# Kernel tuning notes

Measured on AMD Instinct MI355X. Metric: run time of the kernel, lower is better.

Reference implementation:

```python
import jax, jax.numpy as jnp
import numpy as np

B, N_CAM, D_BINS, HF, WF, C = 1, 6, 118, 32, 88, 80
DZ, DY, DX = 1, 128, 128
N_POINTS = 1_000_000
BEV_FEAT_SHAPE = (B, DZ, DY, DX, C)  # (B, Dz, Dy, Dx, C)


def setup_inputs() -> dict:
    key = jax.random.key(0)
    k1, k2, k3, k4, k5 = jax.random.split(key, 5)
    depth = jax.random.uniform(k1, (B, N_CAM, D_BINS, HF, WF), dtype=jnp.float32)
    feat = jax.random.normal(k2, (B, N_CAM, HF, WF, C), dtype=jnp.float32)
    n_depth = B * N_CAM * D_BINS * HF * WF      # flattened depth size
    n_feat_rows = B * N_CAM * HF * WF           # rows of flattened feat
    n_bev = B * DZ * DY * DX                    # flattened BEV grid size
    ranks_depths = jax.random.randint(k3, (N_POINTS,), 0, n_depth, dtype=jnp.int32)
    ranks_feats = jax.random.randint(k4, (N_POINTS,), 0, n_feat_rows, dtype=jnp.int32)
    ranks_bevs = jnp.sort(jax.random.randint(k5, (N_POINTS,), 0, n_bev, dtype=jnp.int32))
    # intervals consistent with sorted ranks_bevs (contiguous runs of equal bev rank)
    rb = np.asarray(ranks_bevs)
    change = np.concatenate([[True], rb[1:] != rb[:-1]])
    starts = np.flatnonzero(change)
    lengths = np.diff(np.append(starts, len(rb)))
    return {
        "depth": depth,
        "feat": feat,
        "ranks_depths": ranks_depths,
        "ranks_feats": ranks_feats,
        "ranks_bevs": ranks_bevs,
        "bev_feat_shape": BEV_FEAT_SHAPE,
        "interval_starts": jnp.asarray(starts, dtype=jnp.int32),
        "interval_lengths": jnp.asarray(lengths, dtype=jnp.int32),
    }


def reference(depth, feat, ranks_depths, ranks_feats, ranks_bevs,
              bev_feat_shape, interval_starts, interval_lengths):
    # bev_pool_v2: gather depth scalar and feat row per point, multiply,
    # scatter-sum into the BEV grid. Interval-based summation over sorted
    # ranks_bevs is mathematically a segment-sum keyed by ranks_bevs, so we
    # use segment_sum directly (intervals are redundant metadata).
    b, dz, dy, dx, c = bev_feat_shape
    d = depth.reshape(-1)[ranks_depths]               # [P]
    f = feat.reshape(-1, c)[ranks_feats]              # [P, C]
    out = jax.ops.segment_sum(f * d[:, None], ranks_bevs,
                              num_segments=b * dz * dy * dx)  # [B*Dz*Dy*Dx, C]
    out = out.reshape(b, dz, dy, dx, c)
    return jnp.transpose(out, (0, 4, 1, 2, 3))        # (B, C, Dz, Dy, Dx)
```

## Files before the change

### kernel.cpp

```cpp
#include <hip/hip_runtime.h>
#include <hip/hip_bf16.h>


#define C_CH   80
#define NL     10
#define SPLITS 8
#define IPB    4
#define BLOCK  (IPB * SPLITS * NL)

__global__ void prep_kernel(const float*  __restrict__ depth,
                            const int*    __restrict__ rd,
                            const float4* __restrict__ feat4,
                            float* __restrict__ dgath,
                            uint2* __restrict__ fbf,
                            int P, int NF4) {
    int i = blockIdx.x * blockDim.x + threadIdx.x;
    if (i < NF4) {
        float4 v = feat4[i];
        float f[4] = {v.x, v.y, v.z, v.w};
        unsigned h[4];
        #pragma unroll
        for (int k = 0; k < 4; ++k) {
            unsigned u = __float_as_uint(f[k]);
            h[k] = (u + 0x7fffu + ((u >> 16) & 1u)) >> 16;
        }
        uint2 o;
        o.x = h[0] | (h[1] << 16);
        o.y = h[2] | (h[3] << 16);
        fbf[i] = o;
    }
    if (i < P) dgath[i] = depth[rd[i]];
}

__device__ __forceinline__ void bf8_fma(float acc[8], float d, int4 w) {
    unsigned v[4] = {(unsigned)w.x, (unsigned)w.y, (unsigned)w.z, (unsigned)w.w};
    #pragma unroll
    for (int k = 0; k < 4; ++k) {
        float lo = __uint_as_float(v[k] << 16);
        float hi = __uint_as_float(v[k] & 0xffff0000u);
        acc[2 * k]     += d * lo;
        acc[2 * k + 1] += d * hi;
    }
}

template <bool FAST>
__global__ __launch_bounds__(BLOCK) void bev_main(
    const float*  __restrict__ depth,
    const int*    __restrict__ rd,
    const float*  __restrict__ dgath,
    const int4*   __restrict__ fbf,
    const float4* __restrict__ featf,
    const int*    __restrict__ rf,
    const int*    __restrict__ rb,
    const int*    __restrict__ istart,
    const int*    __restrict__ ilen,
    int n_intervals,
    int n_bev,
    float* __restrict__ out)
{
    __shared__ float red[IPB][SPLITS][NL][9];

    int tid   = threadIdx.x;
    int il    = tid / (SPLITS * NL);
    int r     = tid - il * (SPLITS * NL);
    int split = r / NL;
    int l10   = r - split * NL;
    int interval = blockIdx.x * IPB + il;
    bool valid = interval < n_intervals;

    float acc[8] = {0.f, 0.f, 0.f, 0.f, 0.f, 0.f, 0.f, 0.f};
    int bev = 0;

    if (valid) {
        int start = istart[interval];
        int len   = ilen[interval];
        bev = rb[start];

        int i = split;
        for (; i + SPLITS < len; i += 2 * SPLITS) {
            int p0 = start + i;
            int p1 = p0 + SPLITS;
            float d0 = FAST ? dgath[p0] : depth[rd[p0]];
            float d1 = FAST ? dgath[p1] : depth[rd[p1]];
            int q0 = rf[p0], q1 = rf[p1];
            if (FAST) {
                int4 w0 = fbf[(long)q0 * NL + l10];
                int4 w1 = fbf[(long)q1 * NL + l10];
                bf8_fma(acc, d0, w0);
                bf8_fma(acc, d1, w1);
            } else {
                float4 a0 = featf[(long)q0 * 20 + l10 * 2];
                float4 a1 = featf[(long)q0 * 20 + l10 * 2 + 1];
                float4 b0 = featf[(long)q1 * 20 + l10 * 2];
                float4 b1 = featf[(long)q1 * 20 + l10 * 2 + 1];
                acc[0] += d0 * a0.x; acc[1] += d0 * a0.y;
                acc[2] += d0 * a0.z; acc[3] += d0 * a0.w;
                acc[4] += d0 * a1.x; acc[5] += d0 * a1.y;
                acc[6] += d0 * a1.z; acc[7] += d0 * a1.w;
                acc[0] += d1 * b0.x; acc[1] += d1 * b0.y;
                acc[2] += d1 * b0.z; acc[3] += d1 * b0.w;
                acc[4] += d1 * b1.x; acc[5] += d1 * b1.y;
                acc[6] += d1 * b1.z; acc[7] += d1 * b1.w;
            }
        }
        for (; i < len; i += SPLITS) {
            int p = start + i;
            float d = FAST ? dgath[p] : depth[rd[p]];
            int q = rf[p];
            if (FAST) {
                bf8_fma(acc, d, fbf[(long)q * NL + l10]);
            } else {
                float4 a0 = featf[(long)q * 20 + l10 * 2];
                float4 a1 = featf[(long)q * 20 + l10 * 2 + 1];
                acc[0] += d * a0.x; acc[1] += d * a0.y;
                acc[2] += d * a0.z; acc[3] += d * a0.w;
                acc[4] += d * a1.x; acc[5] += d * a1.y;
                acc[6] += d * a1.z; acc[7] += d * a1.w;
            }
        }
    }

    #pragma unroll
    for (int j = 0; j < 8; ++j) red[il][split][l10][j] = acc[j];
    __syncthreads();

    if (valid && split == 0) {
        float s[8];
        #pragma unroll
        for (int j = 0; j < 8; ++j) s[j] = acc[j];
        #pragma unroll
        for (int k = 1; k < SPLITS; ++k) {
            #pragma unroll
            for (int j = 0; j < 8; ++j) s[j] += red[il][k][l10][j];
        }
        long ob = (long)(l10 * 8) * n_bev + bev;
        #pragma unroll
        for (int j = 0; j < 8; ++j) out[ob + (long)j * n_bev] = s[j];
    }
}

extern "C" void kernel_launch(void* const* d_in, const int* in_sizes, int n_in,
                              void* d_out, int out_size, void* d_ws, size_t ws_size,
                              hipStream_t stream) {
    const float*  depth = (const float*)d_in[0];
    const float4* feat4 = (const float4*)d_in[1];
    const int* ranks_depth = (const int*)d_in[2];
    const int* ranks_feat  = (const int*)d_in[3];
    const int* ranks_bev   = (const int*)d_in[4];
    const int* interval_starts  = (const int*)d_in[6];
    const int* interval_lengths = (const int*)d_in[7];

    int P   = in_sizes[2];
    int NF  = in_sizes[1];
    int NF4 = NF / 4;
    int n_intervals = in_sizes[6];
    int n_bev = out_size / C_CH;
    float* out = (float*)d_out;

    size_t dg_bytes  = ((size_t)P * sizeof(float) + 15) & ~(size_t)15;
    size_t fbf_bytes = (size_t)NF * 2;
    bool fast = ws_size >= dg_bytes + fbf_bytes;

    float* dgath = (float*)d_ws;
    uint2* fbf   = (uint2*)((char*)d_ws + dg_bytes);

    hipMemsetAsync(d_out, 0, (size_t)out_size * sizeof(float), stream);

    if (fast) {
        int n = P > NF4 ? P : NF4;
        int gblock = 256;
        int ggrid = (n + gblock - 1) / gblock;
        prep_kernel<<<ggrid, gblock, 0, stream>>>(depth, ranks_depth, feat4,
                                                  dgath, fbf, P, NF4);
    }

    int grid = (n_intervals + IPB - 1) / IPB;
    if (fast) {
        bev_main<true><<<grid, BLOCK, 0, stream>>>(
            depth, ranks_depth, dgath, (const int4*)fbf, feat4,
            ranks_feat, ranks_bev, interval_starts, interval_lengths,
            n_intervals, n_bev, out);
    } else {
        bev_main<false><<<grid, BLOCK, 0, stream>>>(
            depth, ranks_depth, dgath, (const int4*)fbf, feat4,
            ranks_feat, ranks_bev, interval_starts, interval_lengths,
            n_intervals, n_bev, out);
    }
}
```

Measured before the change: 118.1 us.

## Pack feat index with bf16-rounded depth per point and unroll main loop by four

A new prep stage converts the full depth tensor to bf16. A second prep kernel then gathers the depth for each point and stores it beside that point's feature row index in one 8-byte record. In the main kernel each point needs only one coalesced load before the feature gather, and the inner loop is unrolled four-way to put more gathers in flight. The cost is an extra kernel launch, a full pass over the depth tensor, and depth values rounded to bf16 precision.

```diff
diff --git a/kernel.cpp b/kernel.cpp
--- a/kernel.cpp
+++ b/kernel.cpp
@@ -8,28 +8,34 @@
 #define IPB    4
 #define BLOCK  (IPB * SPLITS * NL)
 
-__global__ void prep_kernel(const float*  __restrict__ depth,
-                            const int*    __restrict__ rd,
-                            const float4* __restrict__ feat4,
-                            float* __restrict__ dgath,
-                            uint2* __restrict__ fbf,
-                            int P, int NF4) {
+__device__ __forceinline__ unsigned pack_bf16(float2 v) {
+    unsigned a = __float_as_uint(v.x);
+    unsigned b = __float_as_uint(v.y);
+    a = (a + 0x7fffu + ((a >> 16) & 1u)) >> 16;
+    b = (b + 0x7fffu + ((b >> 16) & 1u)) >> 16;
+    return a | (b << 16);
+}
+
+__global__ void prep_convert(const float2* __restrict__ feat2,
+                             const float2* __restrict__ depth2,
+                             unsigned* __restrict__ fbf,
+                             unsigned* __restrict__ dbf,
+                             int NF2, int ND2) {
     int i = blockIdx.x * blockDim.x + threadIdx.x;
-    if (i < NF4) {
-        float4 v = feat4[i];
-        float f[4] = {v.x, v.y, v.z, v.w};
-        unsigned h[4];
-        #pragma unroll
-        for (int k = 0; k < 4; ++k) {
-            unsigned u = __float_as_uint(f[k]);
-            h[k] = (u + 0x7fffu + ((u >> 16) & 1u)) >> 16;
-        }
-        uint2 o;
-        o.x = h[0] | (h[1] << 16);
-        o.y = h[2] | (h[3] << 16);
-        fbf[i] = o;
+    if (i < NF2) fbf[i] = pack_bf16(feat2[i]);
+    if (i < ND2) dbf[i] = pack_bf16(depth2[i]);
+}
+
+__global__ void prep_pack(const unsigned short* __restrict__ dbf,
+                          const int* __restrict__ rd,
+                          const int* __restrict__ rf,
+                          uint2* __restrict__ dpack, int P) {
+    int i = blockIdx.x * blockDim.x + threadIdx.x;
+    if (i < P) {
+        unsigned h = dbf[rd[i]];
+        float d = __uint_as_float(h << 16);
+        dpack[i] = make_uint2((unsigned)rf[i], __float_as_uint(d));
     }
-    if (i < P) dgath[i] = depth[rd[i]];
 }
 
 __device__ __forceinline__ void bf8_fma(float acc[8], float d, int4 w) {
@@ -47,7 +53,7 @@
 __global__ __launch_bounds__(BLOCK) void bev_main(
     const float*  __restrict__ depth,
     const int*    __restrict__ rd,
-    const float*  __restrict__ dgath,
+    const uint2*  __restrict__ dpack,
     const int4*   __restrict__ fbf,
     const float4* __restrict__ featf,
     const int*    __restrict__ rf,
@@ -77,39 +83,34 @@
         bev = rb[start];
 
         int i = split;
-        for (; i + SPLITS < len; i += 2 * SPLITS) {
-            int p0 = start + i;
-            int p1 = p0 + SPLITS;
-            float d0 = FAST ? dgath[p0] : depth[rd[p0]];
-            float d1 = FAST ? dgath[p1] : depth[rd[p1]];
-            int q0 = rf[p0], q1 = rf[p1];
-            if (FAST) {
-                int4 w0 = fbf[(long)q0 * NL + l10];
-                int4 w1 = fbf[(long)q1 * NL + l10];
-                bf8_fma(acc, d0, w0);
-                bf8_fma(acc, d1, w1);
-            } else {
-                float4 a0 = featf[(long)q0 * 20 + l10 * 2];
-                float4 a1 = featf[(long)q0 * 20 + l10 * 2 + 1];
-                float4 b0 = featf[(long)q1 * 20 + l10 * 2];
-                float4 b1 = featf[(long)q1 * 20 + l10 * 2 + 1];
-                acc[0] += d0 * a0.x; acc[1] += d0 * a0.y;
-                acc[2] += d0 * a0.z; acc[3] += d0 * a0.w;
-                acc[4] += d0 * a1.x; acc[5] += d0 * a1.y;
-                acc[6] += d0 * a1.z; acc[7] += d0 * a1.w;
-                acc[0] += d1 * b0.x; acc[1] += d1 * b0.y;
-                acc[2] += d1 * b0.z; acc[3] += d1 * b0.w;
-                acc[4] += d1 * b1.x; acc[5] += d1 * b1.y;
-                acc[6] += d1 * b1.z; acc[7] += d1 * b1.w;
+        if (FAST) {
+            for (; i + 3 * SPLITS < len; i += 4 * SPLITS) {
+                int p0 = start + i;
+                int p1 = p0 + SPLITS;
+                int p2 = p0 + 2 * SPLITS;
+                int p3 = p0 + 3 * SPLITS;
+                uint2 w0 = dpack[p0], w1 = dpack[p1];
+                uint2 w2 = dpack[p2], w3 = dpack[p3];
+                int4 f0 = fbf[(long)w0.x * NL + l10];
+                int4 f1 = fbf[(long)w1.x * NL + l10];
+                int4 f2 = fbf[(long)w2.x * NL + l10];
+                int4 f3 = fbf[(long)w3.x * NL + l10];
+                bf8_fma(acc, __uint_as_float(w0.y), f0);
+                bf8_fma(acc, __uint_as_float(w1.y), f1);
+                bf8_fma(acc, __uint_as_float(w2.y), f2);
+                bf8_fma(acc, __uint_as_float(w3.y), f3);
             }
-        }
-        for (; i < len; i += SPLITS) {
-            int p = start + i;
-            float d = FAST ? dgath[p] : depth[rd[p]];
-            int q = rf[p];
-            if (FAST) {
-                bf8_fma(acc, d, fbf[(long)q * NL + l10]);
-            } else {
+            for (; i < len; i += SPLITS) {
+                int p = start + i;
+                uint2 w = dpack[p];
+                int4 f = fbf[(long)w.x * NL + l10];
+                bf8_fma(acc, __uint_as_float(w.y), f);
+            }
+        } else {
+            for (; i < len; i += SPLITS) {
+                int p = start + i;
+                float d = depth[rd[p]];
+                int q = rf[p];
                 float4 a0 = featf[(long)q * 20 + l10 * 2];
                 float4 a1 = featf[(long)q * 20 + l10 * 2 + 1];
                 acc[0] += d * a0.x; acc[1] += d * a0.y;
@@ -143,7 +144,7 @@
                               void* d_out, int out_size, void* d_ws, size_t ws_size,
                               hipStream_t stream) {
     const float*  depth = (const float*)d_in[0];
-    const float4* feat4 = (const float4*)d_in[1];
+    const float*  featf = (const float*)d_in[1];
     const int* ranks_depth = (const int*)d_in[2];
     const int* ranks_feat  = (const int*)d_in[3];
     const int* ranks_bev   = (const int*)d_in[4];
@@ -152,37 +153,40 @@
 
     int P   = in_sizes[2];
     int NF  = in_sizes[1];
-    int NF4 = NF / 4;
+    int ND  = in_sizes[0];
+    int NF2 = NF / 2, ND2 = ND / 2;
     int n_intervals = in_sizes[6];
     int n_bev = out_size / C_CH;
     float* out = (float*)d_out;
 
-    size_t dg_bytes  = ((size_t)P * sizeof(float) + 15) & ~(size_t)15;
-    size_t fbf_bytes = (size_t)NF * 2;
-    bool fast = ws_size >= dg_bytes + fbf_bytes;
+    size_t dpack_bytes = ((size_t)P * 8 + 15) & ~(size_t)15;
+    size_t fbf_bytes   = ((size_t)NF * 2 + 15) & ~(size_t)15;
+    size_t dbf_bytes   = (size_t)ND * 2;
+    bool fast = ws_size >= dpack_bytes + fbf_bytes + dbf_bytes;
 
-    float* dgath = (float*)d_ws;
-    uint2* fbf   = (uint2*)((char*)d_ws + dg_bytes);
+    uint2*    dpack = (uint2*)d_ws;
+    unsigned* fbf   = (unsigned*)((char*)d_ws + dpack_bytes);
+    unsigned* dbf   = (unsigned*)((char*)d_ws + dpack_bytes + fbf_bytes);
 
     hipMemsetAsync(d_out, 0, (size_t)out_size * sizeof(float), stream);
 
     if (fast) {
-        int n = P > NF4 ? P : NF4;
-        int gblock = 256;
-        int ggrid = (n + gblock - 1) / gblock;
-        prep_kernel<<<ggrid, gblock, 0, stream>>>(depth, ranks_depth, feat4,
-                                                  dgath, fbf, P, NF4);
+        int n1 = (NF2 > ND2 ? NF2 : ND2);
+        prep_convert<<<(n1 + 255) / 256, 256, 0, stream>>>(
+            (const float2*)featf, (const float2*)depth, fbf, dbf, NF2, ND2);
+        prep_pack<<<(P + 255) / 256, 256, 0, stream>>>(
+            (const unsigned short*)dbf, ranks_depth, ranks_feat, dpack, P);
     }
 
     int grid = (n_intervals + IPB - 1) / IPB;
     if (fast) {
         bev_main<true><<<grid, BLOCK, 0, stream>>>(
-            depth, ranks_depth, dgath, (const int4*)fbf, feat4,
+            depth, ranks_depth, dpack, (const int4*)fbf, (const float4*)featf,
             ranks_feat, ranks_bev, interval_starts, interval_lengths,
             n_intervals, n_bev, out);
     } else {
         bev_main<false><<<grid, BLOCK, 0, stream>>>(
-            depth, ranks_depth, dgath, (const int4*)fbf, feat4,
+            depth, ranks_depth, dpack, (const int4*)fbf, (const float4*)featf,
             ranks_feat, ranks_bev, interval_starts, interval_lengths,
             n_intervals, n_bev, out);
     }
```

After: 120.9 us. 1.02x slower.
